# Performance work log

Hardware: AMD Instinct MI355X
Metric: run time of the kernel (lower is better)

## Reference

```python
import jax, jax.numpy as jnp
import numpy as np

PH, PW = 16, 16
EMBED_DIM = 768

def setup_inputs() -> dict:
    key = jax.random.key(0)
    k1, k2, k3, k4, k5 = jax.random.split(key, 5)
    B, C, H, W = 32, 3, 384, 384
    N = 576
    x = jax.random.normal(k1, (B, C, H, W), dtype=jnp.float32)
    h_idx = jax.random.randint(k2, (B, N), 0, H - PH, dtype=jnp.int32)
    w_idx = jax.random.randint(k3, (B, N), 0, W - PW, dtype=jnp.int32)
    in_feat = PH * PW * C
    # nn.Linear default init: U(-1/sqrt(in), 1/sqrt(in))
    bound = 1.0 / np.sqrt(in_feat)
    proj_w = jax.random.uniform(k4, (EMBED_DIM, in_feat), jnp.float32, -bound, bound)
    proj_b = jax.random.uniform(k5, (EMBED_DIM,), jnp.float32, -bound, bound)
    return {"x": x, "h_idx": h_idx, "w_idx": w_idx, "proj_w": proj_w, "proj_b": proj_b}

def reference(x, h_idx, w_idx, proj_w, proj_b):
    # x: [B, C, H, W]; h_idx, w_idx: [B, N]
    B, C, H, W = x.shape
    N = h_idx.shape[1]
    rows = h_idx[:, :, None] + jnp.arange(PH, dtype=h_idx.dtype)   # [B, N, PH]
    cols = w_idx[:, :, None] + jnp.arange(PW, dtype=w_idx.dtype)   # [B, N, PW]
    xt = jnp.transpose(x, (0, 2, 3, 1))                            # [B, H, W, C]
    b_ix = jnp.arange(B)[:, None, None, None]
    # gather patches: [B, N, PH, PW, C]
    patches = xt[b_ix, rows[:, :, :, None], cols[:, :, None, :], :]
    # match torch flatten order (C, PH, PW)
    patches = jnp.transpose(patches, (0, 1, 4, 2, 3)).reshape(B, N, C * PH * PW)
    # linear projection: [B, N, E]
    return jnp.einsum('bnf,ef->bne', patches, proj_w) + proj_b
```

## Files before the change

kernel.cpp:

```cpp
#include <hip/hip_runtime.h>
#include <hip/hip_bf16.h>
#include <stdint.h>

#define B_   32
#define C_   3
#define H_   384
#define W_   384
#define N_   576
#define ED   768
#define KF   768
#define M_   (B_ * N_)

typedef __attribute__((ext_vector_type(8))) short   short8;
typedef __attribute__((ext_vector_type(8))) unsigned short ushort8;
typedef __attribute__((ext_vector_type(4))) float   f32x4;

__device__ __forceinline__ unsigned short f2bf(float f) {
    union { float f; unsigned int u; } v; v.f = f;
    unsigned int u = v.u;
    return (unsigned short)((u + 0x7FFFu + ((u >> 16) & 1u)) >> 16);
}

__global__ __launch_bounds__(256) void gather_patches(
    const float* __restrict__ x, const int* __restrict__ h_idx,
    const int* __restrict__ w_idx, unsigned short* __restrict__ Aws) {
    int gid = blockIdx.x * 256 + threadIdx.x;
    int m   = gid / 96;
    int kb  = gid - m * 96;
    int k0  = kb * 8;
    int b   = m / N_;
    int c   = k0 >> 8;
    int rem = k0 & 255;
    int ph  = rem >> 4;
    int pw  = rem & 15;
    int h = h_idx[m] + ph;
    int w = w_idx[m] + pw;
    const float* src = x + (((b * C_ + c) * H_ + h) * (long)W_ + w);
    ushort8 o;
#pragma unroll
    for (int i = 0; i < 8; ++i) o[i] = f2bf(src[i]);
    *(ushort8*)(Aws + (size_t)m * KF + k0) = o;
}

__global__ __launch_bounds__(256) void conv_w(
    const float* __restrict__ w, unsigned short* __restrict__ Wb) {
    int gid = blockIdx.x * 256 + threadIdx.x;
    const float4* s = (const float4*)w + (size_t)gid * 2;
    float4 a = s[0], bq = s[1];
    ushort8 o;
    o[0] = f2bf(a.x);  o[1] = f2bf(a.y);  o[2] = f2bf(a.z);  o[3] = f2bf(a.w);
    o[4] = f2bf(bq.x); o[5] = f2bf(bq.y); o[6] = f2bf(bq.z); o[7] = f2bf(bq.w);
    *(ushort8*)(Wb + (size_t)gid * 8) = o;
}

#define GLD16(g, l)                                                        \
    __builtin_amdgcn_global_load_lds(                                      \
        (const __attribute__((address_space(1))) unsigned int*)(g),        \
        (__attribute__((address_space(3))) unsigned int*)(l), 16, 0, 0)

#define BK 64

__global__ __launch_bounds__(256) void gemm_bt(
    const unsigned short* __restrict__ A, const unsigned short* __restrict__ Wb,
    const float* __restrict__ bias, float* __restrict__ out) {
    __shared__ unsigned short sA[128 * BK];
    __shared__ unsigned short sB[128 * BK];

    const int t = threadIdx.x;

    const int lin = blockIdx.y * 6 + blockIdx.x;
    const int swz = (lin & 7) * 108 + (lin >> 3);
    const int m0  = (swz / 6) * 128;
    const int e0  = (swz % 6) * 128;

    const int lane = t & 63;
    const int wid  = t >> 6;
    const int wr   = wid >> 1;
    const int wc   = wid & 1;
    const int r16  = lane & 15;
    const int kh   = lane >> 4;

    f32x4 acc[4][4];
#pragma unroll
    for (int i = 0; i < 4; ++i)
#pragma unroll
        for (int j = 0; j < 4; ++j) acc[i][j] = (f32x4)0.0f;

    int st_row[4], st_gc[4];
#pragma unroll
    for (int r = 0; r < 4; ++r) {
        const int o   = r * 4096 + t * 16;
        const int row = o >> 7;
        const int s   = (o >> 4) & 7;
        st_row[r] = row;
        st_gc[r]  = (s ^ (row & 7)) * 8;
    }

    for (int kt = 0; kt < KF / BK; ++kt) {
        const int k0 = kt * BK;
#pragma unroll
        for (int r = 0; r < 4; ++r) {
            const int o = r * 4096 + t * 16;
            GLD16(A  + (size_t)(m0 + st_row[r]) * KF + k0 + st_gc[r], (char*)sA + o);
            GLD16(Wb + (size_t)(e0 + st_row[r]) * KF + k0 + st_gc[r], (char*)sB + o);
        }
        __syncthreads();

#pragma unroll
        for (int kk = 0; kk < 2; ++kk) {
            short8 af[4], bf[4];
#pragma unroll
            for (int mi = 0; mi < 4; ++mi) {
                const int ar = wr * 64 + mi * 16 + r16;
                const int sl = ((kk << 2) + kh) ^ (ar & 7);
                af[mi] = *(const short8*)&sA[ar * BK + sl * 8];
            }
#pragma unroll
            for (int ni = 0; ni < 4; ++ni) {
                const int br = wc * 64 + ni * 16 + r16;
                const int sl = ((kk << 2) + kh) ^ (br & 7);
                bf[ni] = *(const short8*)&sB[br * BK + sl * 8];
            }
#pragma unroll
            for (int mi = 0; mi < 4; ++mi)
#pragma unroll
                for (int ni = 0; ni < 4; ++ni)
                    acc[mi][ni] = __builtin_amdgcn_mfma_f32_16x16x32_bf16(
                        af[mi], bf[ni], acc[mi][ni], 0, 0, 0);
        }
        __syncthreads();
    }

#pragma unroll
    for (int mi = 0; mi < 4; ++mi) {
#pragma unroll
        for (int ni = 0; ni < 4; ++ni) {
            const int ge = e0 + wc * 64 + ni * 16 + r16;
            const float bv = bias[ge];
#pragma unroll
            for (int j = 0; j < 4; ++j) {
                const int gm = m0 + wr * 64 + mi * 16 + kh * 4 + j;
                out[(size_t)gm * ED + ge] = acc[mi][ni][j] + bv;
            }
        }
    }
}

extern "C" void kernel_launch(void* const* d_in, const int* in_sizes, int n_in,
                              void* d_out, int out_size, void* d_ws, size_t ws_size,
                              hipStream_t stream) {
    const float* x      = (const float*)d_in[0];
    const int*   h_idx  = (const int*)  d_in[1];
    const int*   w_idx  = (const int*)  d_in[2];
    const float* proj_w = (const float*)d_in[3];
    const float* proj_b = (const float*)d_in[4];
    float*       out    = (float*)d_out;

    unsigned short* Aws = (unsigned short*)d_ws;
    unsigned short* Wws = Aws + (size_t)M_ * KF;

    gather_patches<<<M_ * 96 / 256, 256, 0, stream>>>(x, h_idx, w_idx, Aws);
    conv_w<<<(ED * KF / 8) / 256, 256, 0, stream>>>(proj_w, Wws);
    gemm_bt<<<dim3(ED / 128, M_ / 128), 256, 0, stream>>>(Aws, Wws, proj_b, out);
}
```

Measured before the change: 153.2 us.

## Fuse patch gather and bf16 conversion into the GEMM A-tile load

```diff
diff --git a/kernel.cpp b/kernel.cpp
--- a/kernel.cpp
+++ b/kernel.cpp
@@ -6,6 +6,7 @@
 #define C_   3
 #define H_   384
 #define W_   384
+#define HW_  (H_ * W_)
 #define N_   576
 #define ED   768
 #define KF   768
@@ -14,32 +15,12 @@
 typedef __attribute__((ext_vector_type(8))) short   short8;
 typedef __attribute__((ext_vector_type(8))) unsigned short ushort8;
 typedef __attribute__((ext_vector_type(4))) float   f32x4;
+typedef __attribute__((ext_vector_type(4))) unsigned int uint4v;
 
 __device__ __forceinline__ unsigned short f2bf(float f) {
     union { float f; unsigned int u; } v; v.f = f;
     unsigned int u = v.u;
     return (unsigned short)((u + 0x7FFFu + ((u >> 16) & 1u)) >> 16);
-}
-
-__global__ __launch_bounds__(256) void gather_patches(
-    const float* __restrict__ x, const int* __restrict__ h_idx,
-    const int* __restrict__ w_idx, unsigned short* __restrict__ Aws) {
-    int gid = blockIdx.x * 256 + threadIdx.x;
-    int m   = gid / 96;
-    int kb  = gid - m * 96;
-    int k0  = kb * 8;
-    int b   = m / N_;
-    int c   = k0 >> 8;
-    int rem = k0 & 255;
-    int ph  = rem >> 4;
-    int pw  = rem & 15;
-    int h = h_idx[m] + ph;
-    int w = w_idx[m] + pw;
-    const float* src = x + (((b * C_ + c) * H_ + h) * (long)W_ + w);
-    ushort8 o;
-#pragma unroll
-    for (int i = 0; i < 8; ++i) o[i] = f2bf(src[i]);
-    *(ushort8*)(Aws + (size_t)m * KF + k0) = o;
 }
 
 __global__ __launch_bounds__(256) void conv_w(
@@ -60,8 +41,13 @@
 
 #define BK 64
 
-__global__ __launch_bounds__(256) void gemm_bt(
-    const unsigned short* __restrict__ A, const unsigned short* __restrict__ Wb,
+__device__ __forceinline__ unsigned int pkbf(unsigned int hi, unsigned int lo) {
+    return __builtin_amdgcn_perm(hi, lo, 0x07060302);
+}
+
+__global__ __launch_bounds__(256) void gemm_fused(
+    const float* __restrict__ x, const int* __restrict__ h_idx,
+    const int* __restrict__ w_idx, const unsigned short* __restrict__ Wb,
     const float* __restrict__ bias, float* __restrict__ out) {
     __shared__ unsigned short sA[128 * BK];
     __shared__ unsigned short sB[128 * BK];
@@ -80,11 +66,20 @@
     const int r16  = lane & 15;
     const int kh   = lane >> 4;
 
-    f32x4 acc[4][4];
-#pragma unroll
-    for (int i = 0; i < 4; ++i)
-#pragma unroll
-        for (int j = 0; j < 4; ++j) acc[i][j] = (f32x4)0.0f;
+    const int m_loc = t & 127;
+    const int p0    = t >> 7;
+    const int m     = m0 + m_loc;
+    const int bb    = m / N_;
+    const int h     = h_idx[m];
+    const int w     = w_idx[m];
+    const float* xb = x + (size_t)(bb * C_) * HW_ + (size_t)h * W_ + w;
+    const int m7 = m_loc & 7;
+    char* sAb = (char*)sA;
+    const int rb  = m_loc * 128;
+    const int a00 = rb + (((2 * p0    ) ^ m7) << 4);
+    const int a01 = rb + (((2 * p0 + 1) ^ m7) << 4);
+    const int a10 = rb + (((2 * p0 + 4) ^ m7) << 4);
+    const int a11 = rb + (((2 * p0 + 5) ^ m7) << 4);
 
     int st_row[4], st_gc[4];
 #pragma unroll
@@ -96,13 +91,55 @@
         st_gc[r]  = (s ^ (row & 7)) * 8;
     }
 
+    f32x4 acc[4][4];
+#pragma unroll
+    for (int i = 0; i < 4; ++i)
+#pragma unroll
+        for (int j = 0; j < 4; ++j) acc[i][j] = (f32x4)0.0f;
+
     for (int kt = 0; kt < KF / BK; ++kt) {
-        const int k0 = kt * BK;
-#pragma unroll
-        for (int r = 0; r < 4; ++r) {
-            const int o = r * 4096 + t * 16;
-            GLD16(A  + (size_t)(m0 + st_row[r]) * KF + k0 + st_gc[r], (char*)sA + o);
-            GLD16(Wb + (size_t)(e0 + st_row[r]) * KF + k0 + st_gc[r], (char*)sB + o);
+        const int k0  = kt * BK;
+        const int c   = kt >> 2;
+        const int ph0 = (kt & 3) * 4;
+
+#pragma unroll
+        for (int r = 0; r < 4; ++r)
+            GLD16(Wb + (size_t)(e0 + st_row[r]) * KF + k0 + st_gc[r],
+                  (char*)sB + r * 4096 + t * 16);
+
+        const float* r0p = xb + (size_t)c * HW_ + (size_t)(ph0 + p0) * W_;
+        const float* r1p = r0p + 2 * W_;
+        {
+            float fv[16];
+            __builtin_memcpy(fv, r0p, 64);
+            unsigned int u[16];
+#pragma unroll
+            for (int i = 0; i < 16; ++i) {
+                union { float f; unsigned int u; } cv; cv.f = fv[i];
+                u[i] = cv.u + 0x8000u;
+            }
+            uint4v lo = { pkbf(u[1], u[0]), pkbf(u[3], u[2]),
+                          pkbf(u[5], u[4]), pkbf(u[7], u[6]) };
+            uint4v hi = { pkbf(u[9], u[8]),  pkbf(u[11], u[10]),
+                          pkbf(u[13], u[12]), pkbf(u[15], u[14]) };
+            *(uint4v*)(sAb + a00) = lo;
+            *(uint4v*)(sAb + a01) = hi;
+        }
+        {
+            float fv[16];
+            __builtin_memcpy(fv, r1p, 64);
+            unsigned int u[16];
+#pragma unroll
+            for (int i = 0; i < 16; ++i) {
+                union { float f; unsigned int u; } cv; cv.f = fv[i];
+                u[i] = cv.u + 0x8000u;
+            }
+            uint4v lo = { pkbf(u[1], u[0]), pkbf(u[3], u[2]),
+                          pkbf(u[5], u[4]), pkbf(u[7], u[6]) };
+            uint4v hi = { pkbf(u[9], u[8]),  pkbf(u[11], u[10]),
+                          pkbf(u[13], u[12]), pkbf(u[15], u[14]) };
+            *(uint4v*)(sAb + a10) = lo;
+            *(uint4v*)(sAb + a11) = hi;
         }
         __syncthreads();
 
@@ -156,10 +193,9 @@
     const float* proj_b = (const float*)d_in[4];
     float*       out    = (float*)d_out;
 
-    unsigned short* Aws = (unsigned short*)d_ws;
-    unsigned short* Wws = Aws + (size_t)M_ * KF;
-
-    gather_patches<<<M_ * 96 / 256, 256, 0, stream>>>(x, h_idx, w_idx, Aws);
+    unsigned short* Wws = (unsigned short*)d_ws;
+
     conv_w<<<(ED * KF / 8) / 256, 256, 0, stream>>>(proj_w, Wws);
-    gemm_bt<<<dim3(ED / 128, M_ / 128), 256, 0, stream>>>(Aws, Wws, proj_b, out);
-}
+    gemm_fused<<<dim3(ED / 128, M_ / 128), 256, 0, stream>>>(
+        x, h_idx, w_idx, Wws, proj_b, out);
+}
```

Measured after the change: 167.1 us. +9.1%, slower.
